# Performance work log

Measured on AMD Instinct MI355X. Metric: run time of the kernel, lower is better.

The kernel has to match this reference:

```python
import jax, jax.numpy as jnp
import numpy as np

B, H, W = 64, 256, 256
G = 64
V = G * G          # 4096
HID = 512
S = 50


def _conv(x, w, b):
    # x: (B,C,H,W), w: (O,I,3,3) -> 'same' conv, NCHW
    y = jax.lax.conv_general_dilated(x, w, (1, 1), 'SAME',
                                     dimension_numbers=('NCHW', 'OIHW', 'NCHW'))
    return y + b[None, :, None, None]


def setup_inputs() -> dict:
    key = jax.random.key(0)
    ks = jax.random.split(key, 14)

    def lin(k, shape, fan_in):
        return (jax.random.normal(k, shape, jnp.float32) / np.float32(np.sqrt(fan_in)))

    return {
        'mask': jax.random.uniform(ks[0], (B, 1, H, W), jnp.float32),
        'target_ids': jax.random.randint(ks[1], (B, S), 0, V),
        'conv1_w': lin(ks[2], (16, 1, 3, 3), 9), 'conv1_b': jnp.zeros((16,), jnp.float32),
        'conv2_w': lin(ks[3], (32, 16, 3, 3), 16 * 9), 'conv2_b': jnp.zeros((32,), jnp.float32),
        'feat_w': lin(ks[4], (HID, 32), 32), 'feat_b': jnp.zeros((HID,), jnp.float32),
        'ctx_w': lin(ks[5], (HID, HID), HID), 'ctx_b': jnp.zeros((HID,), jnp.float32),
        'tok_emb': jax.random.normal(ks[6], (V + 1, HID), jnp.float32) * 0.02,
        'w_ih': lin(ks[7], (4 * HID, HID), HID), 'w_hh': lin(ks[8], (4 * HID, HID), HID),
        'b_ih': jnp.zeros((4 * HID,), jnp.float32), 'b_hh': jnp.zeros((4 * HID,), jnp.float32),
        'head_w': lin(ks[9], (V, HID), HID), 'head_b': jnp.zeros((V,), jnp.float32),
    }


def reference(mask, target_ids, conv1_w, conv1_b, conv2_w, conv2_b,
              feat_w, feat_b, ctx_w, ctx_b, tok_emb,
              w_ih, w_hh, b_ih, b_hh, head_w, head_b):
    b = mask.shape[0]
    vocab = head_w.shape[0]

    # --- CNN encoder ---
    x = jax.nn.relu(_conv(mask, conv1_w, conv1_b))                    # (B,16,H,W)
    x = jax.lax.reduce_window(x, -jnp.inf, jax.lax.max,
                              (1, 1, 2, 2), (1, 1, 2, 2), 'VALID')    # (B,16,H/2,W/2)
    x = jax.nn.relu(_conv(x, conv2_w, conv2_b))                       # (B,32,H/2,W/2)
    x = x.mean(axis=(2, 3))                                           # AdaptiveAvgPool2d(1) -> (B,32)

    h0 = x @ feat_w.T + feat_b                                        # (B,HID)
    c0 = jnp.zeros_like(h0)
    ctx = h0 @ ctx_w.T + ctx_b                                        # (B,HID)

    # Full teacher forcing (ratio=1.0): input token at t=0 is start token V,
    # at t>0 it is target_ids[:, t-1]. All embeddings gathered upfront.
    start = jnp.full((b, 1), vocab, dtype=target_ids.dtype)
    toks = jnp.concatenate([start, target_ids[:, :-1]], axis=1)       # (B,S)
    embs = tok_emb[toks]                                              # (B,S,HID)
    lstm_in = jnp.swapaxes(embs, 0, 1) + ctx[None]                    # (S,B,HID)

    bias = b_ih + b_hh

    def step(carry, inp):
        h, c = carry
        gates = inp @ w_ih.T + h @ w_hh.T + bias                      # (B,4*HID)
        i, f, g, o = jnp.split(gates, 4, axis=-1)
        c = jax.nn.sigmoid(f) * c + jax.nn.sigmoid(i) * jnp.tanh(g)
        h = jax.nn.sigmoid(o) * jnp.tanh(c)
        logit = h @ head_w.T + head_b                                 # (B,V)
        return (h, c), logit

    _, logits = jax.lax.scan(step, (h0, c0), lstm_in)                 # (S,B,V)
    return jnp.swapaxes(logits, 0, 1)                                 # (B,S,V)
```

## Files before the change

kernel.cpp:

```cpp
#include <hip/hip_runtime.h>
#include <cmath>

typedef __attribute__((ext_vector_type(8))) _Float16 f16x8;
typedef __attribute__((ext_vector_type(4))) float f32x4;
typedef __attribute__((ext_vector_type(4))) unsigned u32x4;

#define LSTM_NB 32

__device__ __forceinline__ unsigned short f2h(float x) {
  return __builtin_bit_cast(unsigned short, (_Float16)x);
}

__device__ __forceinline__ void h2f2(unsigned u, float& a, float& b) {
  a = (float)__builtin_bit_cast(_Float16, (unsigned short)(u & 0xffffu));
  b = (float)__builtin_bit_cast(_Float16, (unsigned short)(u >> 16));
}

__device__ __forceinline__ void gload16(const void* g, void* l) {
  __builtin_amdgcn_global_load_lds(
      (const __attribute__((address_space(1))) void*)g,
      (__attribute__((address_space(3))) void*)l, 16, 0, 0);
}

__device__ __forceinline__ void cload16(const void* p, u32x4* dst) {
  asm volatile("global_load_dwordx4 %0, %1, off sc0 sc1"
               : "=v"(*dst)
               : "v"(p));
}

__global__ __launch_bounds__(512) void k_conv(
    const float* __restrict__ mask, const float* __restrict__ w1,
    const float* __restrict__ b1, const float* __restrict__ w2,
    const float* __restrict__ b2, float* __restrict__ part)
{
  __shared__ unsigned short s_p1[16][18 * 36];
  __shared__ float s_w1[144];
  __shared__ float s_b1[16];
  __shared__ float s_w2[4608];
  __shared__ float s_b2[32];

  const int tid = threadIdx.x;
  const int b = blockIdx.x >> 5;
  const int tile = blockIdx.x & 31;
  const int px0 = (tile & 3) * 32, py0 = (tile >> 2) * 16;
  const float* mb = mask + (size_t)b * 65536;

  for (int i = tid; i < 144; i += 512) s_w1[i] = w1[i];
  for (int i = tid; i < 4608; i += 512) s_w2[i] = w2[i];
  if (tid < 16) s_b1[tid] = b1[tid];
  if (tid < 32) s_b2[tid] = b2[tid];
  __syncthreads();

  for (int idx = tid; idx < 18 * 34; idx += 512) {
    int ly = idx / 34, lx = idx - ly * 34;
    int py = py0 - 1 + ly, px = px0 - 1 + lx;
    if (py < 0 || py >= 128 || px < 0 || px >= 128) {
      for (int o = 0; o < 16; o++) s_p1[o][ly * 36 + lx] = 0;
    } else {
      float patch[4][4];
      int gy0 = 2 * py - 1, gx0 = 2 * px - 1;
#pragma unroll
      for (int i = 0; i < 4; i++) {
        int gy = gy0 + i;
        bool yok = (gy >= 0 && gy < 256);
#pragma unroll
        for (int j = 0; j < 4; j++) {
          int gx = gx0 + j;
          patch[i][j] = (yok && gx >= 0 && gx < 256) ? mb[gy * 256 + gx] : 0.f;
        }
      }
      for (int o = 0; o < 16; o++) {
        float m = 0.f;
#pragma unroll
        for (int dy = 0; dy < 2; dy++)
#pragma unroll
          for (int dx = 0; dx < 2; dx++) {
            float v = s_b1[o];
#pragma unroll
            for (int ky = 0; ky < 3; ky++)
#pragma unroll
              for (int kx = 0; kx < 3; kx++)
                v = fmaf(patch[dy + ky][dx + kx], s_w1[o * 9 + ky * 3 + kx], v);
            m = fmaxf(m, v);
          }
        s_p1[o][ly * 36 + lx] = f2h(m);
      }
    }
  }
  __syncthreads();

  const int ocg = tid >> 6;
  const int sp = tid & 63;
  const int sx = (sp & 7) * 4, sy = (sp >> 3) * 2;
  float acc[4][8];
#pragma unroll
  for (int a = 0; a < 4; a++)
#pragma unroll
    for (int q = 0; q < 8; q++) acc[a][q] = 0.f;

  for (int ic = 0; ic < 16; ic++) {
    float p[4][6];
#pragma unroll
    for (int i = 0; i < 4; i++) {
      const unsigned short* row = &s_p1[ic][(sy + i) * 36 + sx];
      unsigned u0 = *(const unsigned*)(row);
      unsigned u1 = *(const unsigned*)(row + 2);
      unsigned u2 = *(const unsigned*)(row + 4);
      h2f2(u0, p[i][0], p[i][1]);
      h2f2(u1, p[i][2], p[i][3]);
      h2f2(u2, p[i][4], p[i][5]);
    }
#pragma unroll
    for (int o4 = 0; o4 < 4; o4++) {
      const int oc = ocg * 4 + o4;
      const float* w = &s_w2[(oc * 16 + ic) * 9];
      float w00 = w[0], w01 = w[1], w02 = w[2];
      float w10 = w[3], w11 = w[4], w12 = w[5];
      float w20 = w[6], w21 = w[7], w22 = w[8];
#pragma unroll
      for (int y = 0; y < 2; y++)
#pragma unroll
        for (int x = 0; x < 4; x++) {
          float s = acc[o4][y * 4 + x];
          s = fmaf(p[y][x], w00, s);
          s = fmaf(p[y][x + 1], w01, s);
          s = fmaf(p[y][x + 2], w02, s);
          s = fmaf(p[y + 1][x], w10, s);
          s = fmaf(p[y + 1][x + 1], w11, s);
          s = fmaf(p[y + 1][x + 2], w12, s);
          s = fmaf(p[y + 2][x], w20, s);
          s = fmaf(p[y + 2][x + 1], w21, s);
          s = fmaf(p[y + 2][x + 2], w22, s);
          acc[o4][y * 4 + x] = s;
        }
    }
  }

  const int lane = tid & 63;
#pragma unroll
  for (int o4 = 0; o4 < 4; o4++) {
    float bv = s_b2[ocg * 4 + o4];
    float s = 0.f;
#pragma unroll
    for (int q = 0; q < 8; q++) s += fmaxf(acc[o4][q] + bv, 0.f);
    for (int off = 32; off > 0; off >>= 1) s += __shfl_down(s, off, 64);
    if (lane == 0) part[(b * 32 + tile) * 32 + ocg * 4 + o4] = s;
  }
}

__global__ __launch_bounds__(256) void k_pool_ctx(
    const float* __restrict__ part, const float* __restrict__ feat_w,
    const float* __restrict__ feat_b, const float* __restrict__ ctx_w,
    const float* __restrict__ ctx_b, float* __restrict__ h0,
    unsigned short* __restrict__ h0f, float* __restrict__ ctx)
{
  const int b = blockIdx.x, tid = threadIdx.x;
  __shared__ float pl[32];
  __shared__ float hs[512];
  if (tid < 32) {
    float s = 0.f;
    for (int t = 0; t < 32; t++) s += part[(b * 32 + t) * 32 + tid];
    pl[tid] = s * (1.0f / 16384.0f);
  }
  __syncthreads();
  for (int j = tid; j < 512; j += 256) {
    float acc = feat_b[j];
    const float* w = feat_w + j * 32;
#pragma unroll
    for (int ic = 0; ic < 32; ic++) acc = fmaf(pl[ic], w[ic], acc);
    h0[b * 512 + j] = acc;
    h0f[b * 512 + j] = f2h(acc);
    hs[j] = acc;
  }
  __syncthreads();
  for (int j = tid; j < 512; j += 256) {
    const float* w = ctx_w + (size_t)j * 512;
    float s0 = 0.f, s1 = 0.f, s2 = 0.f, s3 = 0.f;
    for (int k = 0; k < 512; k += 4) {
      float4 w4 = *(const float4*)(w + k);
      s0 = fmaf(hs[k], w4.x, s0);
      s1 = fmaf(hs[k + 1], w4.y, s1);
      s2 = fmaf(hs[k + 2], w4.z, s2);
      s3 = fmaf(hs[k + 3], w4.w, s3);
    }
    ctx[b * 512 + j] = ctx_b[j] + ((s0 + s1) + (s2 + s3));
  }
}

__global__ __launch_bounds__(256) void k_prep(
    const float* __restrict__ wih, const float* __restrict__ hw,
    unsigned short* __restrict__ wihb, unsigned short* __restrict__ hwb,
    int* __restrict__ cnt)
{
  const int i = blockIdx.x * 256 + threadIdx.x;
  if (i < 64) cnt[i] = 0;
  if (i < 262144) {
    float4 v = *(const float4*)(wih + (size_t)i * 4);
    unsigned lo = (unsigned)f2h(v.x) | ((unsigned)f2h(v.y) << 16);
    unsigned hi = (unsigned)f2h(v.z) | ((unsigned)f2h(v.w) << 16);
    *(uint2*)(wihb + (size_t)i * 4) = make_uint2(lo, hi);
  } else if (i < 786432) {
    const int j = i - 262144;
    float4 v = *(const float4*)(hw + (size_t)j * 4);
    unsigned lo = (unsigned)f2h(v.x) | ((unsigned)f2h(v.y) << 16);
    unsigned hi = (unsigned)f2h(v.z) | ((unsigned)f2h(v.w) << 16);
    *(uint2*)(hwb + (size_t)j * 4) = make_uint2(lo, hi);
  }
}

__global__ __launch_bounds__(256) void k_zero_f(float* __restrict__ p) {
  p[blockIdx.x * 256 + threadIdx.x] = 0.f;
}

__global__ __launch_bounds__(128) void k_build_A(
    const float* __restrict__ tok_emb, const int* __restrict__ tgt,
    const float* __restrict__ ctx, unsigned short* __restrict__ A)
{
  const int r = blockIdx.x;
  const int t = r >> 6, b = r & 63;
  const int tok = (t == 0) ? 4096 : tgt[b * 50 + (t - 1)];
  const int i = threadIdx.x * 4;
  float4 ev = *(const float4*)(tok_emb + (size_t)tok * 512 + i);
  float4 cv = *(const float4*)(ctx + b * 512 + i);
  unsigned lo = (unsigned)f2h(ev.x + cv.x) | ((unsigned)f2h(ev.y + cv.y) << 16);
  unsigned hi = (unsigned)f2h(ev.z + cv.z) | ((unsigned)f2h(ev.w + cv.w) << 16);
  *(uint2*)(A + (size_t)r * 512 + i) = make_uint2(lo, hi);
}

template <int MODE>
__global__ __launch_bounds__(256) void k_gemm_mfma(
    const unsigned short* __restrict__ A, const unsigned short* __restrict__ B,
    const float* __restrict__ bias_a, const float* __restrict__ bias_b,
    float* __restrict__ C, int NB)
{
  __shared__ unsigned short sA[128 * 32];
  __shared__ unsigned short sB[128 * 32];
  const int tid = threadIdx.x;
  const int bx = blockIdx.x % NB, by = blockIdx.x / NB;
  const int lane = tid & 63, wv = tid >> 6;
  const int wr = wv >> 1, wc = wv & 1;
  const unsigned short* Ab = A + (size_t)by * 128 * 512;
  const unsigned short* Bb = B + (size_t)bx * 128 * 512;

  f32x4 acc[4][4];
#pragma unroll
  for (int m = 0; m < 4; m++)
#pragma unroll
    for (int n = 0; n < 4; n++) acc[m][n] = (f32x4){0.f, 0.f, 0.f, 0.f};

  const int r0 = tid >> 2, c0 = (tid & 3) * 8;
  const int idx1 = tid + 256;
  const int r1 = idx1 >> 2, c1 = (idx1 & 3) * 8;
  unsigned short* lA0 = sA + (size_t)wv * 512;
  unsigned short* lA1 = sA + 2048 + (size_t)wv * 512;
  unsigned short* lB0 = sB + (size_t)wv * 512;
  unsigned short* lB1 = sB + 2048 + (size_t)wv * 512;

  const int frow = lane & 15;
  const int foff = (lane >> 4) * 8;

  for (int kc = 0; kc < 512; kc += 32) {
    gload16(Ab + (size_t)r0 * 512 + kc + c0, lA0);
    gload16(Ab + (size_t)r1 * 512 + kc + c1, lA1);
    gload16(Bb + (size_t)r0 * 512 + kc + c0, lB0);
    gload16(Bb + (size_t)r1 * 512 + kc + c1, lB1);
    __syncthreads();

    f16x8 af[4], bfr[4];
#pragma unroll
    for (int m = 0; m < 4; m++)
      af[m] = *(const f16x8*)(sA + (wr * 64 + m * 16 + frow) * 32 + foff);
#pragma unroll
    for (int n = 0; n < 4; n++)
      bfr[n] = *(const f16x8*)(sB + (wc * 64 + n * 16 + frow) * 32 + foff);
#pragma unroll
    for (int m = 0; m < 4; m++)
#pragma unroll
      for (int n = 0; n < 4; n++)
        acc[m][n] = __builtin_amdgcn_mfma_f32_16x16x32_f16(
            af[m], bfr[n], acc[m][n], 0, 0, 0);
    __syncthreads();
  }

#pragma unroll
  for (int n = 0; n < 4; n++) {
    const int gc = bx * 128 + wc * 64 + n * 16 + (lane & 15);
    const float bv = (MODE == 0) ? (bias_a[gc] + bias_b[gc]) : bias_a[gc];
#pragma unroll
    for (int m = 0; m < 4; m++) {
      const int rb = by * 128 + wr * 64 + m * 16 + (lane >> 4) * 4;
#pragma unroll
      for (int j = 0; j < 4; j++) {
        const int r = rb + j;
        float v = acc[m][n][j] + bv;
        int t = r >> 6, bb = r & 63;
        if (MODE == 0) {
          C[(size_t)t * 131072 + (size_t)gc * 64 + bb] = v;
        } else {
          C[((size_t)bb * 50 + t) * 4096 + gc] = v;
        }
      }
    }
  }
}

__global__ __launch_bounds__(256, 1) void k_lstm_mfma(
    const float* __restrict__ xgT,
    const float* __restrict__ w_hh,
    const unsigned short* __restrict__ h0f,
    unsigned short* __restrict__ hallf,
    int* __restrict__ cnt)
{
  __shared__ unsigned short s_h[64 * 512];
  __shared__ float s_g[4][64][17];
  const int tid = threadIdx.x;
  const int kb = blockIdx.x;
  const int g = tid >> 6;
  const int lane = tid & 63;
  const int frow = lane & 15;
  const int foff = (lane >> 4) * 8;

  f16x8 wf[16];
  {
    const float* wrow = w_hh + (size_t)(g * 512 + kb * 16 + frow) * 512;
#pragma unroll
    for (int kf = 0; kf < 16; kf++) {
      float tmp[8];
      *(float4*)tmp = *(const float4*)(wrow + kf * 32 + foff);
      *(float4*)(tmp + 4) = *(const float4*)(wrow + kf * 32 + foff + 4);
#pragma unroll
      for (int j = 0; j < 8; j++) wf[kf][j] = (_Float16)tmp[j];
    }
  }

  float c[4] = {0.f, 0.f, 0.f, 0.f};
  const int b2 = tid & 63, dd2 = tid >> 6;

  for (int t = 0; t < 50; ++t) {
    const unsigned short* H = t ? hallf + (size_t)(t - 1) * 32768 : h0f;

    const float* xr =
        xgT + (size_t)t * 131072 + (size_t)(kb * 16 + dd2 * 4) * 64 + b2;
    float xv[16];
#pragma unroll
    for (int gq = 0; gq < 4; gq++)
#pragma unroll
      for (int i = 0; i < 4; i++)
        xv[gq * 4 + i] = xr[(size_t)(gq * 512 + i) * 64];

    {
      u32x4 r[16];
#pragma unroll
      for (int i = 0; i < 16; i++)
        cload16((const char*)H + (size_t)(tid + i * 256) * 16, &r[i]);
      asm volatile("s_waitcnt vmcnt(0)" ::: "memory");
      __builtin_amdgcn_sched_barrier(0);
#pragma unroll
      for (int i = 0; i < 16; i++) {
        int byte = (tid + i * 256) * 16;
        int swz = byte ^ (((byte >> 10) & 7) << 4);
        *(u32x4*)((char*)s_h + swz) = r[i];
      }
    }
    __syncthreads();

    f32x4 acc[4];
#pragma unroll
    for (int mt = 0; mt < 4; mt++) acc[mt] = (f32x4){0.f, 0.f, 0.f, 0.f};
#pragma unroll
    for (int kf = 0; kf < 16; kf++) {
#pragma unroll
      for (int mt = 0; mt < 4; mt++) {
        const int row = mt * 16 + frow;
        const int byte = (row << 10) + kf * 64 + foff * 2;
        const int swz = byte ^ ((row & 7) << 4);
        f16x8 ah = *(const f16x8*)((const char*)s_h + swz);
        acc[mt] =
            __builtin_amdgcn_mfma_f32_16x16x32_f16(ah, wf[kf], acc[mt], 0, 0, 0);
      }
    }
#pragma unroll
    for (int mt = 0; mt < 4; mt++)
#pragma unroll
      for (int j = 0; j < 4; j++)
        s_g[g][mt * 16 + (lane >> 4) * 4 + j][frow] = acc[mt][j];
    __syncthreads();

    unsigned long long qf = 0;
#pragma unroll
    for (int i = 0; i < 4; i++) {
      float gi = s_g[0][b2][dd2 * 4 + i] + xv[0 + i];
      float gf = s_g[1][b2][dd2 * 4 + i] + xv[4 + i];
      float gg = s_g[2][b2][dd2 * 4 + i] + xv[8 + i];
      float go = s_g[3][b2][dd2 * 4 + i] + xv[12 + i];
      float ig = 1.f / (1.f + expf(-gi));
      float fg = 1.f / (1.f + expf(-gf));
      float og = 1.f / (1.f + expf(-go));
      float gt = tanhf(gg);
      c[i] = fmaf(fg, c[i], ig * gt);
      float h = og * tanhf(c[i]);
      qf |= (unsigned long long)f2h(h) << (16 * i);
    }
    const size_t ho = (size_t)b2 * 512 + kb * 16 + dd2 * 4;
    __hip_atomic_store((unsigned long long*)(hallf + (size_t)t * 32768 + ho),
                       qf, __ATOMIC_RELAXED, __HIP_MEMORY_SCOPE_AGENT);
    __syncthreads();
    if (tid == 0) {
      __hip_atomic_fetch_add(&cnt[t], 1, __ATOMIC_RELAXED,
                             __HIP_MEMORY_SCOPE_AGENT);
      while (__hip_atomic_load(&cnt[t], __ATOMIC_RELAXED,
                               __HIP_MEMORY_SCOPE_AGENT) < LSTM_NB) {
        __builtin_amdgcn_s_sleep(1);
      }
    }
    __syncthreads();
  }
}

__global__ __launch_bounds__(256) void k_lstm_step1(
    const float* __restrict__ xgT, const float* __restrict__ w_hh,
    const float* __restrict__ hin, float* __restrict__ hout,
    unsigned short* __restrict__ hallf_t, float* __restrict__ cbuf, int t)
{
  __shared__ float s_w[8][512];
  __shared__ float s_g[2][4][64];
  const int tid = threadIdx.x;
  const int dd0 = blockIdx.x * 2;

  for (int idx = tid; idx < 1024; idx += 256) {
    int row = idx >> 7;
    int k4 = (idx & 127) << 2;
    int q_ = row >> 1, dd_i = row & 1;
    *(float4*)&s_w[row][k4] =
        *(const float4*)(w_hh + (size_t)(q_ * 512 + dd0 + dd_i) * 512 + k4);
  }
  const int b = tid & 63;
  const int q = tid >> 6;
  __syncthreads();

  const float* hc = hin + b * 512;
  const float* xr = xgT + (size_t)t * 131072 + (size_t)(q * 512 + dd0) * 64 + b;
  float a0 = xr[0], a1 = xr[64];
  const float* w0 = s_w[q * 2 + 0];
  const float* w1 = s_w[q * 2 + 1];
#pragma unroll 8
  for (int k = 0; k < 512; k += 4) {
    float4 h4 = *(const float4*)(hc + k);
    float4 u = *(const float4*)(w0 + k);
    float4 v = *(const float4*)(w1 + k);
    a0 = fmaf(h4.x, u.x, fmaf(h4.y, u.y, fmaf(h4.z, u.z, fmaf(h4.w, u.w, a0))));
    a1 = fmaf(h4.x, v.x, fmaf(h4.y, v.y, fmaf(h4.z, v.z, fmaf(h4.w, v.w, a1))));
  }
  s_g[0][q][b] = a0;
  s_g[1][q][b] = a1;
  __syncthreads();
  if (q < 2) {
    const int dd = dd0 + q;
    float gi = s_g[q][0][b], gf = s_g[q][1][b];
    float gg = s_g[q][2][b], go = s_g[q][3][b];
    float ig = 1.f / (1.f + expf(-gi));
    float fg = 1.f / (1.f + expf(-gf));
    float og = 1.f / (1.f + expf(-go));
    float gt = tanhf(gg);
    float c = fmaf(fg, cbuf[b * 512 + dd], ig * gt);
    float h = og * tanhf(c);
    cbuf[b * 512 + dd] = c;
    hout[b * 512 + dd] = h;
    hallf_t[(size_t)b * 512 + dd] = f2h(h);
  }
}

extern "C" void kernel_launch(void* const* d_in, const int* in_sizes, int n_in,
                              void* d_out, int out_size, void* d_ws,
                              size_t ws_size, hipStream_t stream) {
  const float* mask   = (const float*)d_in[0];
  const int*   tgt    = (const int*)d_in[1];
  const float* w1     = (const float*)d_in[2];
  const float* b1     = (const float*)d_in[3];
  const float* w2     = (const float*)d_in[4];
  const float* b2     = (const float*)d_in[5];
  const float* feat_w = (const float*)d_in[6];
  const float* feat_b = (const float*)d_in[7];
  const float* ctx_w  = (const float*)d_in[8];
  const float* ctx_b  = (const float*)d_in[9];
  const float* temb   = (const float*)d_in[10];
  const float* w_ih   = (const float*)d_in[11];
  const float* w_hh_p = (const float*)d_in[12];
  const float* b_ih   = (const float*)d_in[13];
  const float* b_hh   = (const float*)d_in[14];
  const float* head_w = (const float*)d_in[15];
  const float* head_b = (const float*)d_in[16];

  float* ws = (float*)d_ws;
  float* part  = ws;
  float* hbuf  = ws + 65536;
  float* ctx   = ws + 131072;
  int*   cnt   = (int*)(ws + 163840);
  unsigned short* h0f  = (unsigned short*)(ws + 163904);
  unsigned short* Ab16 = (unsigned short*)(ws + 180288);
  unsigned short* hallf = Ab16;
  unsigned short* wihb = (unsigned short*)(ws + 999488);
  unsigned short* hwb  = (unsigned short*)(ws + 1523776);
  float* xgT   = ws + 2572352;
  float* cbuf  = part;
  float* out   = (float*)d_out;

  k_conv<<<2048, 512, 0, stream>>>(mask, w1, b1, w2, b2, part);
  k_prep<<<3072, 256, 0, stream>>>(w_ih, head_w, wihb, hwb, cnt);
  k_pool_ctx<<<64, 256, 0, stream>>>(part, feat_w, feat_b, ctx_w, ctx_b,
                                     hbuf, h0f, ctx);
  k_build_A<<<3200, 128, 0, stream>>>(temb, tgt, ctx, Ab16);
  k_gemm_mfma<0><<<25 * 16, 256, 0, stream>>>(Ab16, wihb, b_ih, b_hh, xgT, 16);

  {
    const float* xgT_c = xgT;
    const float* whh_c = w_hh_p;
    const unsigned short* h0f_c = h0f;
    unsigned short* hallf_c = hallf;
    int* cnt_c = cnt;
    void* args[] = {(void*)&xgT_c, (void*)&whh_c, (void*)&h0f_c,
                    (void*)&hallf_c, (void*)&cnt_c};
    hipError_t e = hipLaunchCooperativeKernel(
        (const void*)k_lstm_mfma, dim3(LSTM_NB), dim3(256), args, 0, stream);
    if (e != hipSuccess) {
      (void)hipGetLastError();
      k_zero_f<<<128, 256, 0, stream>>>(cbuf);
      for (int t = 0; t < 50; t++) {
        const float* hin = hbuf + (t & 1) * 32768;
        float* hout = hbuf + ((t + 1) & 1) * 32768;
        k_lstm_step1<<<256, 256, 0, stream>>>(
            xgT, w_hh_p, hin, hout, hallf + (size_t)t * 32768, cbuf, t);
      }
    }
  }

  k_gemm_mfma<1><<<25 * 32, 256, 0, stream>>>(hallf, hwb, head_b, nullptr, out, 32);
}
```

Measured before the change: 545.2 us.

## Use packed fp16 dot2 in conv2 and per-block flags for LSTM step sync

The second conv now packs pairs of input channels and weights as fp16 and accumulates with packed dot2 instructions into fp32, halving the FMA count and skipping the unpack from half to float. The LSTM cooperative kernel replaces its per-step counter barrier, where every block increments and spins until all arrive, with per-block ready flags. Each step, 32 threads each poll one producer's flag from the previous step before loading h. This moves the wait to just before the dependent load and removes the atomic add contention. It costs more flag memory (1600 ints zeroed in prep) and reduces conv2 accumulation precision to fp16 products.

```diff
diff --git a/kernel.cpp b/kernel.cpp
--- a/kernel.cpp
+++ b/kernel.cpp
@@ -2,6 +2,7 @@
 #include <cmath>
 
 typedef __attribute__((ext_vector_type(8))) _Float16 f16x8;
+typedef __attribute__((ext_vector_type(2))) _Float16 f16x2;
 typedef __attribute__((ext_vector_type(4))) float f32x4;
 typedef __attribute__((ext_vector_type(4))) unsigned u32x4;
 
@@ -11,9 +12,14 @@
   return __builtin_bit_cast(unsigned short, (_Float16)x);
 }
 
-__device__ __forceinline__ void h2f2(unsigned u, float& a, float& b) {
-  a = (float)__builtin_bit_cast(_Float16, (unsigned short)(u & 0xffffu));
-  b = (float)__builtin_bit_cast(_Float16, (unsigned short)(u >> 16));
+__device__ __forceinline__ float dot2(unsigned a, unsigned b, float c) {
+#if __has_builtin(__builtin_amdgcn_fdot2)
+  return __builtin_amdgcn_fdot2(__builtin_bit_cast(f16x2, a),
+                                __builtin_bit_cast(f16x2, b), c, false);
+#else
+  f16x2 av = __builtin_bit_cast(f16x2, a), bv = __builtin_bit_cast(f16x2, b);
+  return fmaf((float)av[0], (float)bv[0], fmaf((float)av[1], (float)bv[1], c));
+#endif
 }
 
 __device__ __forceinline__ void gload16(const void* g, void* l) {
@@ -33,10 +39,10 @@
     const float* __restrict__ b1, const float* __restrict__ w2,
     const float* __restrict__ b2, float* __restrict__ part)
 {
-  __shared__ unsigned short s_p1[16][18 * 36];
+  __shared__ unsigned s_p1p[8][18 * 36];
+  __shared__ unsigned s_w2p[32][8][9];
   __shared__ float s_w1[144];
   __shared__ float s_b1[16];
-  __shared__ float s_w2[4608];
   __shared__ float s_b2[32];
 
   const int tid = threadIdx.x;
@@ -46,7 +52,12 @@
   const float* mb = mask + (size_t)b * 65536;
 
   for (int i = tid; i < 144; i += 512) s_w1[i] = w1[i];
-  for (int i = tid; i < 4608; i += 512) s_w2[i] = w2[i];
+  for (int i = tid; i < 2304; i += 512) {
+    int oc = i / 72, p8 = (i % 72) / 9, k = i % 9;
+    unsigned lo = f2h(w2[(size_t)(oc * 16 + 2 * p8) * 9 + k]);
+    unsigned hi = f2h(w2[(size_t)(oc * 16 + 2 * p8 + 1) * 9 + k]);
+    s_w2p[oc][p8][k] = lo | (hi << 16);
+  }
   if (tid < 16) s_b1[tid] = b1[tid];
   if (tid < 32) s_b2[tid] = b2[tid];
   __syncthreads();
@@ -55,7 +66,7 @@
     int ly = idx / 34, lx = idx - ly * 34;
     int py = py0 - 1 + ly, px = px0 - 1 + lx;
     if (py < 0 || py >= 128 || px < 0 || px >= 128) {
-      for (int o = 0; o < 16; o++) s_p1[o][ly * 36 + lx] = 0;
+      for (int p8 = 0; p8 < 8; p8++) s_p1p[p8][ly * 36 + lx] = 0;
     } else {
       float patch[4][4];
       int gy0 = 2 * py - 1, gx0 = 2 * px - 1;
@@ -69,8 +80,9 @@
           patch[i][j] = (yok && gx >= 0 && gx < 256) ? mb[gy * 256 + gx] : 0.f;
         }
       }
+      float m[16];
       for (int o = 0; o < 16; o++) {
-        float m = 0.f;
+        float mm = 0.f;
 #pragma unroll
         for (int dy = 0; dy < 2; dy++)
 #pragma unroll
@@ -81,10 +93,14 @@
 #pragma unroll
               for (int kx = 0; kx < 3; kx++)
                 v = fmaf(patch[dy + ky][dx + kx], s_w1[o * 9 + ky * 3 + kx], v);
-            m = fmaxf(m, v);
+            mm = fmaxf(mm, v);
           }
-        s_p1[o][ly * 36 + lx] = f2h(m);
-      }
+        m[o] = mm;
+      }
+#pragma unroll
+      for (int p8 = 0; p8 < 8; p8++)
+        s_p1p[p8][ly * 36 + lx] =
+            (unsigned)f2h(m[2 * p8]) | ((unsigned)f2h(m[2 * p8 + 1]) << 16);
     }
   }
   __syncthreads();
@@ -98,39 +114,34 @@
 #pragma unroll
     for (int q = 0; q < 8; q++) acc[a][q] = 0.f;
 
-  for (int ic = 0; ic < 16; ic++) {
-    float p[4][6];
+  for (int p8 = 0; p8 < 8; p8++) {
+    unsigned pp[4][6];
 #pragma unroll
     for (int i = 0; i < 4; i++) {
-      const unsigned short* row = &s_p1[ic][(sy + i) * 36 + sx];
-      unsigned u0 = *(const unsigned*)(row);
-      unsigned u1 = *(const unsigned*)(row + 2);
-      unsigned u2 = *(const unsigned*)(row + 4);
-      h2f2(u0, p[i][0], p[i][1]);
-      h2f2(u1, p[i][2], p[i][3]);
-      h2f2(u2, p[i][4], p[i][5]);
+      const unsigned* row = &s_p1p[p8][(sy + i) * 36 + sx];
+#pragma unroll
+      for (int j = 0; j < 6; j++) pp[i][j] = row[j];
     }
 #pragma unroll
     for (int o4 = 0; o4 < 4; o4++) {
-      const int oc = ocg * 4 + o4;
-      const float* w = &s_w2[(oc * 16 + ic) * 9];
-      float w00 = w[0], w01 = w[1], w02 = w[2];
-      float w10 = w[3], w11 = w[4], w12 = w[5];
-      float w20 = w[6], w21 = w[7], w22 = w[8];
+      const unsigned* w = &s_w2p[ocg * 4 + o4][p8][0];
+      unsigned w00 = w[0], w01 = w[1], w02 = w[2];
+      unsigned w10 = w[3], w11 = w[4], w12 = w[5];
+      unsigned w20 = w[6], w21 = w[7], w22 = w[8];
 #pragma unroll
       for (int y = 0; y < 2; y++)
 #pragma unroll
         for (int x = 0; x < 4; x++) {
           float s = acc[o4][y * 4 + x];
-          s = fmaf(p[y][x], w00, s);
-          s = fmaf(p[y][x + 1], w01, s);
-          s = fmaf(p[y][x + 2], w02, s);
-          s = fmaf(p[y + 1][x], w10, s);
-          s = fmaf(p[y + 1][x + 1], w11, s);
-          s = fmaf(p[y + 1][x + 2], w12, s);
-          s = fmaf(p[y + 2][x], w20, s);
-          s = fmaf(p[y + 2][x + 1], w21, s);
-          s = fmaf(p[y + 2][x + 2], w22, s);
+          s = dot2(pp[y][x], w00, s);
+          s = dot2(pp[y][x + 1], w01, s);
+          s = dot2(pp[y][x + 2], w02, s);
+          s = dot2(pp[y + 1][x], w10, s);
+          s = dot2(pp[y + 1][x + 1], w11, s);
+          s = dot2(pp[y + 1][x + 2], w12, s);
+          s = dot2(pp[y + 2][x], w20, s);
+          s = dot2(pp[y + 2][x + 1], w21, s);
+          s = dot2(pp[y + 2][x + 2], w22, s);
           acc[o4][y * 4 + x] = s;
         }
     }
@@ -190,10 +201,10 @@
 __global__ __launch_bounds__(256) void k_prep(
     const float* __restrict__ wih, const float* __restrict__ hw,
     unsigned short* __restrict__ wihb, unsigned short* __restrict__ hwb,
-    int* __restrict__ cnt)
+    int* __restrict__ flags)
 {
   const int i = blockIdx.x * 256 + threadIdx.x;
-  if (i < 64) cnt[i] = 0;
+  if (i < 1600) flags[i] = 0;
   if (i < 262144) {
     float4 v = *(const float4*)(wih + (size_t)i * 4);
     unsigned lo = (unsigned)f2h(v.x) | ((unsigned)f2h(v.y) << 16);
@@ -309,7 +320,7 @@
     const float* __restrict__ w_hh,
     const unsigned short* __restrict__ h0f,
     unsigned short* __restrict__ hallf,
-    int* __restrict__ cnt)
+    int* __restrict__ flags)
 {
   __shared__ unsigned short s_h[64 * 512];
   __shared__ float s_g[4][64][17];
@@ -347,6 +358,14 @@
 #pragma unroll
       for (int i = 0; i < 4; i++)
         xv[gq * 4 + i] = xr[(size_t)(gq * 512 + i) * 64];
+
+    if (t > 0 && tid < 32) {
+      while (__hip_atomic_load(&flags[(t - 1) * 32 + tid], __ATOMIC_RELAXED,
+                               __HIP_MEMORY_SCOPE_AGENT) == 0) {
+        __builtin_amdgcn_s_sleep(1);
+      }
+    }
+    __syncthreads();
 
     {
       u32x4 r[16];
@@ -405,15 +424,9 @@
     __hip_atomic_store((unsigned long long*)(hallf + (size_t)t * 32768 + ho),
                        qf, __ATOMIC_RELAXED, __HIP_MEMORY_SCOPE_AGENT);
     __syncthreads();
-    if (tid == 0) {
-      __hip_atomic_fetch_add(&cnt[t], 1, __ATOMIC_RELAXED,
-                             __HIP_MEMORY_SCOPE_AGENT);
-      while (__hip_atomic_load(&cnt[t], __ATOMIC_RELAXED,
-                               __HIP_MEMORY_SCOPE_AGENT) < LSTM_NB) {
-        __builtin_amdgcn_s_sleep(1);
-      }
-    }
-    __syncthreads();
+    if (t < 49 && tid == 0)
+      __hip_atomic_store(&flags[t * 32 + kb], 1, __ATOMIC_RELAXED,
+                         __HIP_MEMORY_SCOPE_AGENT);
   }
 }
 
@@ -495,18 +508,18 @@
   float* part  = ws;
   float* hbuf  = ws + 65536;
   float* ctx   = ws + 131072;
-  int*   cnt   = (int*)(ws + 163840);
-  unsigned short* h0f  = (unsigned short*)(ws + 163904);
-  unsigned short* Ab16 = (unsigned short*)(ws + 180288);
+  int*   flags = (int*)(ws + 163840);
+  unsigned short* h0f  = (unsigned short*)(ws + 165440);
+  unsigned short* Ab16 = (unsigned short*)(ws + 181824);
   unsigned short* hallf = Ab16;
-  unsigned short* wihb = (unsigned short*)(ws + 999488);
-  unsigned short* hwb  = (unsigned short*)(ws + 1523776);
-  float* xgT   = ws + 2572352;
+  unsigned short* wihb = (unsigned short*)(ws + 1001024);
+  unsigned short* hwb  = (unsigned short*)(ws + 1525312);
+  float* xgT   = ws + 2573888;
   float* cbuf  = part;
   float* out   = (float*)d_out;
 
   k_conv<<<2048, 512, 0, stream>>>(mask, w1, b1, w2, b2, part);
-  k_prep<<<3072, 256, 0, stream>>>(w_ih, head_w, wihb, hwb, cnt);
+  k_prep<<<3072, 256, 0, stream>>>(w_ih, head_w, wihb, hwb, flags);
   k_pool_ctx<<<64, 256, 0, stream>>>(part, feat_w, feat_b, ctx_w, ctx_b,
                                      hbuf, h0f, ctx);
   k_build_A<<<3200, 128, 0, stream>>>(temb, tgt, ctx, Ab16);
@@ -517,9 +530,9 @@
     const float* whh_c = w_hh_p;
     const unsigned short* h0f_c = h0f;
     unsigned short* hallf_c = hallf;
-    int* cnt_c = cnt;
+    int* flags_c = flags;
     void* args[] = {(void*)&xgT_c, (void*)&whh_c, (void*)&h0f_c,
-                    (void*)&hallf_c, (void*)&cnt_c};
+                    (void*)&hallf_c, (void*)&flags_c};
     hipError_t e = hipLaunchCooperativeKernel(
         (const void*)k_lstm_mfma, dim3(LSTM_NB), dim3(256), args, 0, stream);
     if (e != hipSuccess) {
```

After: 510.6 us. -6.3%, faster.
